# Kernel tuning notes

Hardware: AMD Instinct MI355X
Metric: run time of the kernel (lower is better)

## Reference

```python
import jax, jax.numpy as jnp
import numpy as np
from jax import lax

C = 16
HID = 128
ALIVE_THRESHOLD = 0.1


def _filters(channels):
    sobel_x = jnp.array([[-1, 0, 1], [-2, 0, 2], [-1, 0, 1]], jnp.float32) / 8.0
    sobel_y = jnp.array([[1, 2, 1], [0, 0, 0], [-1, -2, -1]], jnp.float32) / 8.0
    ident = jnp.zeros((3, 3), jnp.float32).at[1, 1].set(1.0)
    # torch: stack -> repeat(channels,1,1) -> unsqueeze(1)  => (3*C, 1, 3, 3), interleaved [id,sx,sy] per channel
    return jnp.tile(jnp.stack([ident, sobel_x, sobel_y]), (channels, 1, 1))[:, None]


def _pad_wrap(x):
    return jnp.pad(x, ((0, 0), (0, 0), (1, 1), (1, 1)), mode='wrap')


def _alive(x_padded, thr):
    # max_pool2d(kernel=3, stride=1, pad=0) on first channel of padded x -> (B,1,H,W)
    m = lax.reduce_window(x_padded[:, :1], -jnp.inf, lax.max,
                          (1, 1, 3, 3), (1, 1, 1, 1), 'VALID')
    return m > thr


def _step(x, w1, b1, w2, filt, channels, thr):
    xp = _pad_wrap(x)
    pre_life = _alive(xp, thr)
    # depthwise conv: each input channel -> [identity, sobel_x, sobel_y] outputs
    delta = lax.conv_general_dilated(
        xp, filt, window_strides=(1, 1), padding='VALID',
        dimension_numbers=('NCHW', 'OIHW', 'NCHW'),
        feature_group_count=channels)  # (B, 3C, H, W)
    h = jax.nn.relu(jnp.einsum('bchw,oc->bohw', delta, w1) + b1[None, :, None, None])
    delta = jnp.einsum('bchw,oc->bohw', h, w2)  # (B, C, H, W)
    x = x + delta
    post_life = _alive(_pad_wrap(x), thr)
    life_mask = (pre_life & post_life).astype(x.dtype)
    return x * life_mask  # alive_threshold > 0 and mass_conserving == 'no'


def setup_inputs() -> dict:
    key = jax.random.key(0)
    k1, k2, k3, k4 = jax.random.split(key, 4)
    x = jax.random.normal(k1, (16, C, 128, 128), jnp.float32)
    w1 = jax.random.normal(k2, (HID, 3 * C), jnp.float32) * (1.0 / np.sqrt(3 * C))
    b1 = jax.random.normal(k3, (HID,), jnp.float32) * 0.01
    w2 = jax.random.normal(k4, (C, HID), jnp.float32) * (1.0 / np.sqrt(HID))
    return {"x": x, "w1": w1, "b1": b1, "w2": w2, "steps": 24}


def reference(x, w1, b1, w2, steps):
    filt = _filters(C)

    def body(carry, _):
        nxt = _step(carry, w1, b1, w2, filt, C, ALIVE_THRESHOLD)
        return nxt, nxt

    _, frames = lax.scan(body, x, None, length=steps)  # (steps, B, C, H, W)
    seq = jnp.concatenate([x[None], frames], axis=0)   # (steps+1, B, C, H, W)
    return jnp.moveaxis(seq, 0, 1)                     # (B, steps+1, C, H, W)
```

## Files before the change

kernel.cpp:

```cpp
#include <hip/hip_runtime.h>
#include <cstdint>

#define B_ 16
#define C_ 16
#define H_ 128
#define W_ 128
#define HID_ 128
#define K_ 48
#define NSTEPS 24
#define THR 0.1f
#define TS 16
#define TP 18
#define FRAMES 25
#define CHW (C_*H_*W_)
#define HW (H_*W_)

__global__ void frame0_copy(const float4* __restrict__ x, float4* __restrict__ out) {
    int idx = blockIdx.x * 256 + threadIdx.x;
    int per_b = CHW / 4;
    int b = idx / per_b;
    int r = idx - b * per_b;
    out[(size_t)b * (FRAMES * CHW / 4) + r] = x[idx];
}

__global__ void w2_transpose(const float* __restrict__ w2, float* __restrict__ w2t) {
    int i = blockIdx.x * 256 + threadIdx.x;
    int c = i >> 7, h = i & 127;
    w2t[h * C_ + c] = w2[i];
}

__global__ __launch_bounds__(256) void stepA(
    const float* __restrict__ frames,
    const float* __restrict__ w1,
    const float* __restrict__ b1,
    const float* __restrict__ w2t,
    float* __restrict__ x1,
    float* __restrict__ premask,
    int s)
{
    __shared__ float xs[C_][TP][TP];
    const int b = blockIdx.z;
    const int ty0 = blockIdx.y * TS, tx0 = blockIdx.x * TS;
    const int tid = threadIdx.x;
    const float* xin = frames + ((size_t)b * FRAMES + s) * CHW;

    for (int p = tid; p < TP * TP; p += 256) {
        int iy = p / TP, ix = p - iy * TP;
        int gy = (ty0 + iy - 1) & (H_ - 1);
        int gx = (tx0 + ix - 1) & (W_ - 1);
        const float* src = xin + gy * W_ + gx;
        #pragma unroll
        for (int c = 0; c < C_; ++c)
            xs[c][iy][ix] = src[c * HW];
    }
    __syncthreads();

    const int ly = tid >> 4, lx = tid & 15;

    float m = -1e30f;
    #pragma unroll
    for (int dy = 0; dy < 3; ++dy)
        #pragma unroll
        for (int dx = 0; dx < 3; ++dx)
            m = fmaxf(m, xs[0][ly + dy][lx + dx]);
    const float pre = (m > THR) ? 1.0f : 0.0f;

    float d[K_];
    #pragma unroll
    for (int c = 0; c < C_; ++c) {
        float a00 = xs[c][ly][lx],     a01 = xs[c][ly][lx + 1],     a02 = xs[c][ly][lx + 2];
        float a10 = xs[c][ly + 1][lx],                              a12 = xs[c][ly + 1][lx + 2];
        float a20 = xs[c][ly + 2][lx], a21 = xs[c][ly + 2][lx + 1], a22 = xs[c][ly + 2][lx + 2];
        float a11 = xs[c][ly + 1][lx + 1];
        d[3 * c]     = a11;
        d[3 * c + 1] = (a02 - a00 + 2.0f * (a12 - a10) + a22 - a20) * 0.125f;
        d[3 * c + 2] = (a00 + 2.0f * a01 + a02 - a20 - 2.0f * a21 - a22) * 0.125f;
    }

    float acc[C_];
    #pragma unroll
    for (int c = 0; c < C_; ++c) acc[c] = 0.0f;

    #pragma unroll 2
    for (int h = 0; h < HID_; ++h) {
        const float* wr = w1 + h * K_;
        float s0 = 0.f, s1 = 0.f, s2 = 0.f, s3 = 0.f;
        #pragma unroll
        for (int k = 0; k < K_; k += 4) {
            s0 = fmaf(wr[k + 0], d[k + 0], s0);
            s1 = fmaf(wr[k + 1], d[k + 1], s1);
            s2 = fmaf(wr[k + 2], d[k + 2], s2);
            s3 = fmaf(wr[k + 3], d[k + 3], s3);
        }
        float hv = fmaxf((s0 + s1) + (s2 + s3) + b1[h], 0.0f);
        const float* wc = w2t + h * C_;
        #pragma unroll
        for (int c = 0; c < C_; ++c) acc[c] = fmaf(wc[c], hv, acc[c]);
    }

    const int y = ty0 + ly, x = tx0 + lx;
    float* xo = x1 + (size_t)b * CHW + y * W_ + x;
    #pragma unroll
    for (int c = 0; c < C_; ++c)
        xo[c * HW] = d[3 * c] + acc[c];
    premask[b * HW + y * W_ + x] = pre;
}

__global__ __launch_bounds__(256) void stepB(
    const float* __restrict__ x1,
    const float* __restrict__ premask,
    float* __restrict__ frames,
    int s)
{
    int idx = blockIdx.x * 256 + threadIdx.x;
    int b = idx >> 14;
    int yx = idx & (HW - 1);
    int y = yx >> 7, x = yx & (W_ - 1);
    const float* c0 = x1 + (size_t)b * CHW;
    float m = -1e30f;
    #pragma unroll
    for (int dy = -1; dy <= 1; ++dy) {
        int gy = (y + dy) & (H_ - 1);
        #pragma unroll
        for (int dx = -1; dx <= 1; ++dx) {
            int gx = (x + dx) & (W_ - 1);
            m = fmaxf(m, c0[gy * W_ + gx]);
        }
    }
    float life = (m > THR && premask[idx] != 0.0f) ? 1.0f : 0.0f;
    const float* xi = x1 + (size_t)b * CHW + yx;
    float* xo = frames + ((size_t)b * FRAMES + s + 1) * CHW + yx;
    #pragma unroll
    for (int c = 0; c < C_; ++c)
        xo[c * HW] = xi[c * HW] * life;
}

extern "C" void kernel_launch(void* const* d_in, const int* in_sizes, int n_in,
                              void* d_out, int out_size, void* d_ws, size_t ws_size,
                              hipStream_t stream)
{
    const float* x  = (const float*)d_in[0];
    const float* w1 = (const float*)d_in[1];
    const float* b1 = (const float*)d_in[2];
    const float* w2 = (const float*)d_in[3];
    float* out = (float*)d_out;

    float* x1      = (float*)d_ws;
    float* premask = (float*)((char*)d_ws + (size_t)B_ * CHW * 4);
    float* w2t     = (float*)((char*)d_ws + (size_t)B_ * CHW * 4 + (size_t)B_ * HW * 4);

    w2_transpose<<<8, 256, 0, stream>>>(w2, w2t);
    frame0_copy<<<(B_ * CHW / 4) / 256, 256, 0, stream>>>((const float4*)x, (float4*)out);

    for (int s = 0; s < NSTEPS; ++s) {
        stepA<<<dim3(W_ / TS, H_ / TS, B_), 256, 0, stream>>>(out, w1, b1, w2t, x1, premask, s);
        stepB<<<(B_ * HW) / 256, 256, 0, stream>>>(x1, premask, out, s);
    }
}
```

Measured before the change: 2.340 ms.

## Compute two pixels per thread with packed float2 FMAs in stepA MLP

Each thread in stepA now handles two pixels 16 columns apart, with the tile widened to 32x16. The perception features and accumulators are held as float2 vectors, so both MLP matmuls can use packed FMA instructions. Each weight load from w1 and w2t is now shared by two pixels, which halves per-pixel weight traffic and instruction count. The cost is higher register pressure, which may lower occupancy, and half as many blocks.

```diff
diff --git a/kernel.cpp b/kernel.cpp
--- a/kernel.cpp
+++ b/kernel.cpp
@@ -6,14 +6,22 @@
 #define H_ 128
 #define W_ 128
 #define HID_ 128
-#define K_ 48
 #define NSTEPS 24
 #define THR 0.1f
-#define TS 16
-#define TP 18
+#define TSX 32
+#define TSY 16
+#define TPX 34
+#define TPY 18
 #define FRAMES 25
 #define CHW (C_*H_*W_)
 #define HW (H_*W_)
+
+typedef float v2f __attribute__((ext_vector_type(2)));
+
+#define VFMA(a,b,c) __builtin_elementwise_fma((a),(b),(c))
+
+#define SETD(D,k,v) do { if ((k)&1) (D)[(k)>>1].y = (v); else (D)[(k)>>1].x = (v); } while(0)
+#define GETD(D,k) (((k)&1) ? (D)[(k)>>1].y : (D)[(k)>>1].x)
 
 __global__ void frame0_copy(const float4* __restrict__ x, float4* __restrict__ out) {
     int idx = blockIdx.x * 256 + threadIdx.x;
@@ -38,14 +46,14 @@
     float* __restrict__ premask,
     int s)
 {
-    __shared__ float xs[C_][TP][TP];
+    __shared__ float xs[C_][TPY][TPX];
     const int b = blockIdx.z;
-    const int ty0 = blockIdx.y * TS, tx0 = blockIdx.x * TS;
+    const int ty0 = blockIdx.y * TSY, tx0 = blockIdx.x * TSX;
     const int tid = threadIdx.x;
     const float* xin = frames + ((size_t)b * FRAMES + s) * CHW;
 
-    for (int p = tid; p < TP * TP; p += 256) {
-        int iy = p / TP, ix = p - iy * TP;
+    for (int p = tid; p < TPY * TPX; p += 256) {
+        int iy = p / TPX, ix = p - iy * TPX;
         int gy = (ty0 + iy - 1) & (H_ - 1);
         int gx = (tx0 + ix - 1) & (W_ - 1);
         const float* src = xin + gy * W_ + gx;
@@ -57,53 +65,92 @@
 
     const int ly = tid >> 4, lx = tid & 15;
 
-    float m = -1e30f;
+    float m0 = -1e30f, m1 = -1e30f;
     #pragma unroll
     for (int dy = 0; dy < 3; ++dy)
         #pragma unroll
-        for (int dx = 0; dx < 3; ++dx)
-            m = fmaxf(m, xs[0][ly + dy][lx + dx]);
-    const float pre = (m > THR) ? 1.0f : 0.0f;
-
-    float d[K_];
+        for (int dx = 0; dx < 3; ++dx) {
+            m0 = fmaxf(m0, xs[0][ly + dy][lx + dx]);
+            m1 = fmaxf(m1, xs[0][ly + dy][lx + 16 + dx]);
+        }
+    const float pre0 = (m0 > THR) ? 1.0f : 0.0f;
+    const float pre1 = (m1 > THR) ? 1.0f : 0.0f;
+
+    v2f D0[24], D1[24];
     #pragma unroll
     for (int c = 0; c < C_; ++c) {
-        float a00 = xs[c][ly][lx],     a01 = xs[c][ly][lx + 1],     a02 = xs[c][ly][lx + 2];
-        float a10 = xs[c][ly + 1][lx],                              a12 = xs[c][ly + 1][lx + 2];
-        float a20 = xs[c][ly + 2][lx], a21 = xs[c][ly + 2][lx + 1], a22 = xs[c][ly + 2][lx + 2];
-        float a11 = xs[c][ly + 1][lx + 1];
-        d[3 * c]     = a11;
-        d[3 * c + 1] = (a02 - a00 + 2.0f * (a12 - a10) + a22 - a20) * 0.125f;
-        d[3 * c + 2] = (a00 + 2.0f * a01 + a02 - a20 - 2.0f * a21 - a22) * 0.125f;
-    }
-
-    float acc[C_];
-    #pragma unroll
-    for (int c = 0; c < C_; ++c) acc[c] = 0.0f;
-
-    #pragma unroll 2
+        {
+            float a00 = xs[c][ly][lx],     a01 = xs[c][ly][lx + 1],     a02 = xs[c][ly][lx + 2];
+            float a10 = xs[c][ly + 1][lx],                              a12 = xs[c][ly + 1][lx + 2];
+            float a20 = xs[c][ly + 2][lx], a21 = xs[c][ly + 2][lx + 1], a22 = xs[c][ly + 2][lx + 2];
+            float a11 = xs[c][ly + 1][lx + 1];
+            SETD(D0, 3 * c,     a11);
+            SETD(D0, 3 * c + 1, (a02 - a00 + 2.0f * (a12 - a10) + a22 - a20) * 0.125f);
+            SETD(D0, 3 * c + 2, (a00 + 2.0f * a01 + a02 - a20 - 2.0f * a21 - a22) * 0.125f);
+        }
+        {
+            int kx = lx + 16;
+            float a00 = xs[c][ly][kx],     a01 = xs[c][ly][kx + 1],     a02 = xs[c][ly][kx + 2];
+            float a10 = xs[c][ly + 1][kx],                              a12 = xs[c][ly + 1][kx + 2];
+            float a20 = xs[c][ly + 2][kx], a21 = xs[c][ly + 2][kx + 1], a22 = xs[c][ly + 2][kx + 2];
+            float a11 = xs[c][ly + 1][kx + 1];
+            SETD(D1, 3 * c,     a11);
+            SETD(D1, 3 * c + 1, (a02 - a00 + 2.0f * (a12 - a10) + a22 - a20) * 0.125f);
+            SETD(D1, 3 * c + 2, (a00 + 2.0f * a01 + a02 - a20 - 2.0f * a21 - a22) * 0.125f);
+        }
+    }
+
+    const v2f* __restrict__ w1v = (const v2f*)w1;
+    const v2f* __restrict__ w2v = (const v2f*)w2t;
+
+    v2f A0[8], A1[8];
+    #pragma unroll
+    for (int j = 0; j < 8; ++j) {
+        A0[j].x = 0.0f; A0[j].y = 0.0f;
+        A1[j].x = 0.0f; A1[j].y = 0.0f;
+    }
+
     for (int h = 0; h < HID_; ++h) {
-        const float* wr = w1 + h * K_;
-        float s0 = 0.f, s1 = 0.f, s2 = 0.f, s3 = 0.f;
-        #pragma unroll
-        for (int k = 0; k < K_; k += 4) {
-            s0 = fmaf(wr[k + 0], d[k + 0], s0);
-            s1 = fmaf(wr[k + 1], d[k + 1], s1);
-            s2 = fmaf(wr[k + 2], d[k + 2], s2);
-            s3 = fmaf(wr[k + 3], d[k + 3], s3);
-        }
-        float hv = fmaxf((s0 + s1) + (s2 + s3) + b1[h], 0.0f);
-        const float* wc = w2t + h * C_;
-        #pragma unroll
-        for (int c = 0; c < C_; ++c) acc[c] = fmaf(wc[c], hv, acc[c]);
-    }
-
-    const int y = ty0 + ly, x = tx0 + lx;
-    float* xo = x1 + (size_t)b * CHW + y * W_ + x;
-    #pragma unroll
-    for (int c = 0; c < C_; ++c)
-        xo[c * HW] = d[3 * c] + acc[c];
-    premask[b * HW + y * W_ + x] = pre;
+        const v2f* wr = w1v + h * 24;
+        v2f s0a, s0b, s1a, s1b;
+        s0a.x = 0.f; s0a.y = 0.f; s0b.x = 0.f; s0b.y = 0.f;
+        s1a.x = 0.f; s1a.y = 0.f; s1b.x = 0.f; s1b.y = 0.f;
+        #pragma unroll
+        for (int j = 0; j < 24; j += 2) {
+            v2f wa = wr[j], wb = wr[j + 1];
+            s0a = VFMA(wa, D0[j],     s0a);
+            s0b = VFMA(wb, D0[j + 1], s0b);
+            s1a = VFMA(wa, D1[j],     s1a);
+            s1b = VFMA(wb, D1[j + 1], s1b);
+        }
+        float bb = b1[h];
+        float hv0 = fmaxf((s0a.x + s0a.y) + (s0b.x + s0b.y) + bb, 0.0f);
+        float hv1 = fmaxf((s1a.x + s1a.y) + (s1b.x + s1b.y) + bb, 0.0f);
+        v2f hp0; hp0.x = hv0; hp0.y = hv0;
+        v2f hp1; hp1.x = hv1; hp1.y = hv1;
+        const v2f* wc = w2v + h * 8;
+        #pragma unroll
+        for (int j = 0; j < 8; ++j) {
+            v2f wcj = wc[j];
+            A0[j] = VFMA(wcj, hp0, A0[j]);
+            A1[j] = VFMA(wcj, hp1, A1[j]);
+        }
+    }
+
+    const int y = ty0 + ly;
+    const int xcol = tx0 + lx;
+    float* xo0 = x1 + (size_t)b * CHW + y * W_ + xcol;
+    float* xo1 = xo0 + 16;
+    #pragma unroll
+    for (int c = 0; c < C_; ++c) {
+        float dd0 = ((c) & 1) ? A0[c >> 1].y : A0[c >> 1].x;
+        float dd1 = ((c) & 1) ? A1[c >> 1].y : A1[c >> 1].x;
+        xo0[c * HW] = GETD(D0, 3 * c) + dd0;
+        xo1[c * HW] = GETD(D1, 3 * c) + dd1;
+    }
+    int pmi = b * HW + y * W_ + xcol;
+    premask[pmi] = pre0;
+    premask[pmi + 16] = pre1;
 }
 
 __global__ __launch_bounds__(256) void stepB(
@@ -153,7 +200,7 @@
     frame0_copy<<<(B_ * CHW / 4) / 256, 256, 0, stream>>>((const float4*)x, (float4*)out);
 
     for (int s = 0; s < NSTEPS; ++s) {
-        stepA<<<dim3(W_ / TS, H_ / TS, B_), 256, 0, stream>>>(out, w1, b1, w2t, x1, premask, s);
+        stepA<<<dim3(W_ / TSX, H_ / TSY, B_), 256, 0, stream>>>(out, w1, b1, w2t, x1, premask, s);
         stepB<<<(B_ * HW) / 256, 256, 0, stream>>>(x1, premask, out, s);
     }
 }
```

Result: slower. 2.684 ms (+14.7%).

## Split hidden dimension across wavefronts with interleaved weights and LDS reduction

Applied to the files above, without the earlier changes.

Each stepA block now covers an 8x8 pixel tile, and its four wavefronts each take a quarter of the 128 hidden units. Partial outputs are reduced through shared memory before the write. w1, w2 and b1 are packed into one interleaved per-hidden-row array, so each hidden unit's weights sit on the same rows and load as uniform scalars. The goal is four times more blocks (better occupancy and load balance) and less weight-fetch overhead, at the cost of redundant stencil loads per wave, extra syncs and an LDS reduction.

```diff
diff --git a/kernel.cpp b/kernel.cpp
--- a/kernel.cpp
+++ b/kernel.cpp
@@ -6,14 +6,12 @@
 #define H_ 128
 #define W_ 128
 #define HID_ 128
-#define K_ 48
 #define NSTEPS 24
 #define THR 0.1f
-#define TS 16
-#define TP 18
 #define FRAMES 25
 #define CHW (C_*H_*W_)
 #define HW (H_*W_)
+#define WSTR 80
 
 __global__ void frame0_copy(const float4* __restrict__ x, float4* __restrict__ out) {
     int idx = blockIdx.x * 256 + threadIdx.x;
@@ -23,87 +21,101 @@
     out[(size_t)b * (FRAMES * CHW / 4) + r] = x[idx];
 }
 
-__global__ void w2_transpose(const float* __restrict__ w2, float* __restrict__ w2t) {
-    int i = blockIdx.x * 256 + threadIdx.x;
-    int c = i >> 7, h = i & 127;
-    w2t[h * C_ + c] = w2[i];
+__global__ void wint_build(const float* __restrict__ w1, const float* __restrict__ b1,
+                           const float* __restrict__ w2, float* __restrict__ wint) {
+    int h = threadIdx.x;
+    float* r = wint + h * WSTR;
+    for (int k = 0; k < 48; ++k) r[k] = w1[h * 48 + k];
+    for (int c = 0; c < 16; ++c) r[48 + c] = w2[c * 128 + h];
+    r[64] = b1[h];
 }
 
 __global__ __launch_bounds__(256) void stepA(
     const float* __restrict__ frames,
-    const float* __restrict__ w1,
-    const float* __restrict__ b1,
-    const float* __restrict__ w2t,
+    const float* __restrict__ wint,
     float* __restrict__ x1,
     float* __restrict__ premask,
     int s)
 {
-    __shared__ float xs[C_][TP][TP];
+    __shared__ float smem[4096];
     const int b = blockIdx.z;
-    const int ty0 = blockIdx.y * TS, tx0 = blockIdx.x * TS;
+    const int ty0 = blockIdx.y * 8, tx0 = blockIdx.x * 8;
     const int tid = threadIdx.x;
+    const int p = tid & 63, wv = tid >> 6;
+    const int py = p >> 3, px = p & 7;
     const float* xin = frames + ((size_t)b * FRAMES + s) * CHW;
 
-    for (int p = tid; p < TP * TP; p += 256) {
-        int iy = p / TP, ix = p - iy * TP;
-        int gy = (ty0 + iy - 1) & (H_ - 1);
-        int gx = (tx0 + ix - 1) & (W_ - 1);
-        const float* src = xin + gy * W_ + gx;
-        #pragma unroll
-        for (int c = 0; c < C_; ++c)
-            xs[c][iy][ix] = src[c * HW];
+    #pragma unroll
+    for (int i0 = 0; i0 < 1792; i0 += 256) {
+        int i = i0 + tid;
+        if (i < 1600) {
+            int c = i / 100;
+            int rem = i - c * 100;
+            int iy = rem / 10, ix = rem - iy * 10;
+            int gy = (ty0 + iy - 1) & (H_ - 1);
+            int gx = (tx0 + ix - 1) & (W_ - 1);
+            smem[i] = xin[c * HW + gy * W_ + gx];
+        }
     }
     __syncthreads();
 
-    const int ly = tid >> 4, lx = tid & 15;
-
+    const int pb = py * 10 + px;
     float m = -1e30f;
     #pragma unroll
     for (int dy = 0; dy < 3; ++dy)
         #pragma unroll
         for (int dx = 0; dx < 3; ++dx)
-            m = fmaxf(m, xs[0][ly + dy][lx + dx]);
-    const float pre = (m > THR) ? 1.0f : 0.0f;
+            m = fmaxf(m, smem[pb + dy * 10 + dx]);
+    if (wv == 0)
+        premask[b * HW + (ty0 + py) * W_ + tx0 + px] = (m > THR) ? 1.0f : 0.0f;
 
-    float d[K_];
+    float d[48];
     #pragma unroll
     for (int c = 0; c < C_; ++c) {
-        float a00 = xs[c][ly][lx],     a01 = xs[c][ly][lx + 1],     a02 = xs[c][ly][lx + 2];
-        float a10 = xs[c][ly + 1][lx],                              a12 = xs[c][ly + 1][lx + 2];
-        float a20 = xs[c][ly + 2][lx], a21 = xs[c][ly + 2][lx + 1], a22 = xs[c][ly + 2][lx + 2];
-        float a11 = xs[c][ly + 1][lx + 1];
+        int base = c * 100 + pb;
+        float a00 = smem[base],      a01 = smem[base + 1],  a02 = smem[base + 2];
+        float a10 = smem[base + 10], a11 = smem[base + 11], a12 = smem[base + 12];
+        float a20 = smem[base + 20], a21 = smem[base + 21], a22 = smem[base + 22];
         d[3 * c]     = a11;
         d[3 * c + 1] = (a02 - a00 + 2.0f * (a12 - a10) + a22 - a20) * 0.125f;
         d[3 * c + 2] = (a00 + 2.0f * a01 + a02 - a20 - 2.0f * a21 - a22) * 0.125f;
     }
 
-    float acc[C_];
+    float acc[16];
     #pragma unroll
-    for (int c = 0; c < C_; ++c) acc[c] = 0.0f;
+    for (int c = 0; c < 16; ++c) acc[c] = 0.0f;
 
+    const float* wb = wint + wv * 32 * WSTR;
     #pragma unroll 2
-    for (int h = 0; h < HID_; ++h) {
-        const float* wr = w1 + h * K_;
+    for (int hh = 0; hh < 32; ++hh) {
+        const float* wr = wb + hh * WSTR;
         float s0 = 0.f, s1 = 0.f, s2 = 0.f, s3 = 0.f;
         #pragma unroll
-        for (int k = 0; k < K_; k += 4) {
+        for (int k = 0; k < 48; k += 4) {
             s0 = fmaf(wr[k + 0], d[k + 0], s0);
             s1 = fmaf(wr[k + 1], d[k + 1], s1);
             s2 = fmaf(wr[k + 2], d[k + 2], s2);
             s3 = fmaf(wr[k + 3], d[k + 3], s3);
         }
-        float hv = fmaxf((s0 + s1) + (s2 + s3) + b1[h], 0.0f);
-        const float* wc = w2t + h * C_;
+        float hv = fmaxf((s0 + s1) + (s2 + s3) + wr[64], 0.0f);
         #pragma unroll
-        for (int c = 0; c < C_; ++c) acc[c] = fmaf(wc[c], hv, acc[c]);
+        for (int c = 0; c < 16; ++c) acc[c] = fmaf(wr[48 + c], hv, acc[c]);
     }
 
-    const int y = ty0 + ly, x = tx0 + lx;
-    float* xo = x1 + (size_t)b * CHW + y * W_ + x;
+    __syncthreads();
     #pragma unroll
-    for (int c = 0; c < C_; ++c)
-        xo[c * HW] = d[3 * c] + acc[c];
-    premask[b * HW + y * W_ + x] = pre;
+    for (int c = 0; c < 16; ++c)
+        smem[((wv * 16 + c) << 6) + p] = acc[c];
+    __syncthreads();
+
+    float* xo = x1 + (size_t)b * CHW + (ty0 + py) * W_ + tx0 + px;
+    #pragma unroll
+    for (int j = 0; j < 4; ++j) {
+        int c = (wv << 2) + j;
+        float v = smem[(c << 6) + p] + smem[((16 + c) << 6) + p]
+                + smem[((32 + c) << 6) + p] + smem[((48 + c) << 6) + p];
+        xo[c * HW] = d[3 * c] + v;
+    }
 }
 
 __global__ __launch_bounds__(256) void stepB(
@@ -147,13 +159,13 @@
 
     float* x1      = (float*)d_ws;
     float* premask = (float*)((char*)d_ws + (size_t)B_ * CHW * 4);
-    float* w2t     = (float*)((char*)d_ws + (size_t)B_ * CHW * 4 + (size_t)B_ * HW * 4);
+    float* wint    = (float*)((char*)d_ws + (size_t)B_ * CHW * 4 + (size_t)B_ * HW * 4);
 
-    w2_transpose<<<8, 256, 0, stream>>>(w2, w2t);
+    wint_build<<<1, 128, 0, stream>>>(w1, b1, w2, wint);
     frame0_copy<<<(B_ * CHW / 4) / 256, 256, 0, stream>>>((const float4*)x, (float4*)out);
 
     for (int s = 0; s < NSTEPS; ++s) {
-        stepA<<<dim3(W_ / TS, H_ / TS, B_), 256, 0, stream>>>(out, w1, b1, w2t, x1, premask, s);
+        stepA<<<dim3(W_ / 8, H_ / 8, B_), 256, 0, stream>>>(out, wint, x1, premask, s);
         stepB<<<(B_ * HW) / 256, 256, 0, stream>>>(x1, premask, out, s);
     }
 }
```

Result: slower. 6.696 ms (+186.1%).
